# Kernel tuning notes

Measured on AMD Instinct MI355X. Metric: run time of the kernel, lower is better.

The kernel has to match this reference:

```python
import jax, jax.numpy as jnp
import numpy as np

N, L, S, H, D = 4, 2048, 2048, 8, 64

def setup_inputs() -> dict:
    key = jax.random.key(0)
    kq, kk, kv = jax.random.split(key, 3)
    queries = jax.random.normal(kq, (N, L, H, D), dtype=jnp.float32)
    keys = jax.random.normal(kk, (N, S, H, D), dtype=jnp.float32)
    values = jax.random.normal(kv, (N, S, H, D), dtype=jnp.float32)
    # q_mask all True (avoids NaN rows, matching torch semantics for valid queries);
    # kv_mask is a valid-prefix mask: first 3/4 of kv positions are valid.
    q_mask = jnp.ones((N, L), dtype=bool)
    kv_mask = jnp.arange(S)[None, :] < (S * 3 // 4)
    kv_mask = jnp.broadcast_to(kv_mask, (N, S))
    return {"queries": queries, "keys": keys, "values": values,
            "q_mask": q_mask, "kv_mask": kv_mask}

def reference(queries, keys, values, q_mask, kv_mask):
    # QK: [N, L, S, H]  (torch does broadcasted mul+sum; einsum is the same math)
    QK = jnp.einsum("nlhd,nshd->nlsh", queries, keys)
    mask = q_mask[:, :, None, None] & kv_mask[:, None, :, None]  # [N,L,S,1]
    QK = jnp.where(mask, QK, -jnp.inf)
    softmax_temp = 1.0 / jnp.sqrt(jnp.asarray(D, queries.dtype))
    A = jax.nn.softmax(softmax_temp * QK, axis=2)  # softmax over S
    # AV: [N, L, H, D]
    return jnp.einsum("nlsh,nshd->nlhd", A, values)
```

## Files before the change

### kernel.cpp

```cpp
#include <hip/hip_runtime.h>
#include <hip/hip_bf16.h>
#include <stdint.h>


namespace {

constexpr int N_ = 4, L_ = 2048, S_ = 2048, H_ = 8, D_ = 64;
constexpr int KVBLK = 64;
constexpr int NT = S_ / KVBLK;
constexpr int TILE_BYTES = 64 * 128;
constexpr float QSC = 0.125f * 1.44269504088896f;

typedef __bf16 bf16x8 __attribute__((ext_vector_type(8)));
typedef __bf16 bf16x4 __attribute__((ext_vector_type(4)));
typedef float f32x4 __attribute__((ext_vector_type(4)));

__device__ inline int swz(int row, int byte_in_row) {
    return row * 128 + (byte_in_row ^ ((row & 7) << 4));
}

__device__ inline bf16x8 cvt8(float4 a, float4 b) {
    bf16x8 r;
    r[0] = (__bf16)a.x; r[1] = (__bf16)a.y; r[2] = (__bf16)a.z; r[3] = (__bf16)a.w;
    r[4] = (__bf16)b.x; r[5] = (__bf16)b.y; r[6] = (__bf16)b.z; r[7] = (__bf16)b.w;
    return r;
}

__device__ inline void gl_lds16(const void* g, void* l) {
    __builtin_amdgcn_global_load_lds(
        (const __attribute__((address_space(1))) unsigned int*)g,
        (__attribute__((address_space(3))) unsigned int*)l, 16, 0, 0);
}

__global__ __launch_bounds__(256)
void prep_kernel(const float* __restrict__ K, const float* __restrict__ V,
                 uint8_t* __restrict__ Kimg, uint8_t* __restrict__ Vimg)
{
    const int bid = blockIdx.x;
    const int t   = bid & (NT - 1);
    const int nh  = bid >> 5;
    const int h   = nh & (H_ - 1);
    const int n   = nh / H_;
    const int tid = threadIdx.x;

    uint8_t* kt = Kimg + (size_t)bid * TILE_BYTES;
    uint8_t* vt = Vimg + (size_t)bid * TILE_BYTES;

    {
        const int r = tid >> 2, seg = tid & 3;
        const float* kp = K + (((size_t)n * S_ + t * 64 + r) * H_ + h) * D_ + seg * 16;
        float4 f0 = ((const float4*)kp)[0];
        float4 f1 = ((const float4*)kp)[1];
        float4 f2 = ((const float4*)kp)[2];
        float4 f3 = ((const float4*)kp)[3];
        *(bf16x8*)(kt + swz(r, seg * 32))      = cvt8(f0, f1);
        *(bf16x8*)(kt + swz(r, seg * 32 + 16)) = cvt8(f2, f3);
    }

    {
        const int vd = tid & 63, vw = tid >> 6;
        const float* vp = V + (((size_t)n * S_ + t * 64 + vw * 16) * H_ + h) * D_ + vd;
        #pragma unroll
        for (int i4 = 0; i4 < 4; ++i4) {
            bf16x4 u;
            u[0] = (__bf16)vp[(size_t)(i4 * 4 + 0) * (H_ * D_)];
            u[1] = (__bf16)vp[(size_t)(i4 * 4 + 1) * (H_ * D_)];
            u[2] = (__bf16)vp[(size_t)(i4 * 4 + 2) * (H_ * D_)];
            u[3] = (__bf16)vp[(size_t)(i4 * 4 + 3) * (H_ * D_)];
            *(bf16x4*)(vt + swz(vd, (vw * 16 + i4 * 4) * 2)) = u;
        }
    }
}

__global__ __launch_bounds__(128, 2)
void fa_kernel(const float* __restrict__ Q, const uint8_t* __restrict__ Kimg,
               const uint8_t* __restrict__ Vimg, const void* __restrict__ kvm_raw,
               float* __restrict__ O)
{
    const int b   = blockIdx.x;
    const int xcd = b & 7;
    const int k_  = b >> 3;
    const int nh  = xcd * 4 + (k_ >> 5);
    const int qt  = k_ & 31;
    const int h   = nh & (H_ - 1);
    const int n   = nh / H_;

    const int tid  = threadIdx.x;
    const int wave = tid >> 6;
    const int lane = tid & 63;
    const int lo   = lane & 15;
    const int hi   = lane >> 4;

    const int q0 = qt * 64 + wave * 32;

    __shared__ __align__(16) unsigned char Klds[2][TILE_BYTES];
    __shared__ __align__(16) unsigned char Vtld[2][TILE_BYTES];
    __shared__ __align__(16) unsigned char Plds[2][32 * 128];

    const uint8_t* k8  = (const uint8_t*)kvm_raw;
    const int*     k32 = (const int*)kvm_raw;
    const bool isb = (k8[1] | k8[2] | k8[3]) != 0;
    const size_t mbase = (size_t)n * S_;
    int cnt = 0;
    if (isb) {
        #pragma unroll
        for (int w = 0; w < 4; ++w) {
            uint2 v = *(const uint2*)(k8 + mbase + w * 512 + lane * 8);
            #pragma unroll
            for (int i = 0; i < 4; ++i) cnt += ((v.x >> (8 * i)) & 0xffu) ? 1 : 0;
            #pragma unroll
            for (int i = 0; i < 4; ++i) cnt += ((v.y >> (8 * i)) & 0xffu) ? 1 : 0;
        }
    } else {
        const int4* p = (const int4*)(k32 + mbase);
        #pragma unroll
        for (int w = 0; w < 4; ++w) {
            int4 a = p[w * 128 + lane * 2];
            int4 c = p[w * 128 + lane * 2 + 1];
            cnt += (a.x != 0) + (a.y != 0) + (a.z != 0) + (a.w != 0)
                 + (c.x != 0) + (c.y != 0) + (c.z != 0) + (c.w != 0);
        }
    }
    #pragma unroll
    for (int off = 1; off < 64; off <<= 1) cnt += __shfl_xor(cnt, off, 64);
    const int plen   = cnt;
    const int ntiles = (plen + KVBLK - 1) / KVBLK;

    bf16x8 qf[2][2];
    #pragma unroll
    for (int sub = 0; sub < 2; ++sub) {
        const float* qp = Q + (((size_t)n * L_ + q0 + sub * 16 + lo) * H_ + h) * D_;
        #pragma unroll
        for (int d0 = 0; d0 < 2; ++d0) {
            float4 a = *(const float4*)(qp + d0 * 32 + hi * 8);
            float4 c = *(const float4*)(qp + d0 * 32 + hi * 8 + 4);
            a.x *= QSC; a.y *= QSC; a.z *= QSC; a.w *= QSC;
            c.x *= QSC; c.y *= QSC; c.z *= QSC; c.w *= QSC;
            qf[sub][d0] = cvt8(a, c);
        }
    }

    bf16x8 ones8;
    #pragma unroll
    for (int j = 0; j < 8; ++j) ones8[j] = (__bf16)1.0f;

    f32x4 acc[2][4];
    f32x4 lacc[2];
    #pragma unroll
    for (int sub = 0; sub < 2; ++sub) {
        #pragma unroll
        for (int dt = 0; dt < 4; ++dt) acc[sub][dt] = f32x4{0.f, 0.f, 0.f, 0.f};
        lacc[sub] = f32x4{0.f, 0.f, 0.f, 0.f};
    }

    const uint8_t* kimg_nh = Kimg + (size_t)nh * NT * TILE_BYTES;
    const uint8_t* vimg_nh = Vimg + (size_t)nh * NT * TILE_BYTES;

    auto stage = [&](int buf, int t) {
        const uint8_t* kt = kimg_nh + (size_t)t * TILE_BYTES;
        const uint8_t* vt = vimg_nh + (size_t)t * TILE_BYTES;
        const int base = wave * 4096;
        #pragma unroll
        for (int i = 0; i < 4; ++i) {
            gl_lds16(kt + base + i * 1024 + lane * 16, &Klds[buf][base + i * 1024]);
            gl_lds16(vt + base + i * 1024 + lane * 16, &Vtld[buf][base + i * 1024]);
        }
    };

    if (ntiles > 0) stage(0, 0);

    for (int t = 0; t < ntiles; ++t) {
        const int buf = t & 1;
        const int s0 = t * KVBLK;

        __syncthreads();
        if (t + 1 < ntiles) stage(buf ^ 1, t + 1);

        f32x4 sacc[2][4];
        #pragma unroll
        for (int sub = 0; sub < 2; ++sub)
            #pragma unroll
            for (int nt = 0; nt < 4; ++nt) sacc[sub][nt] = f32x4{0.f, 0.f, 0.f, 0.f};
        #pragma unroll
        for (int nt = 0; nt < 4; ++nt) {
            #pragma unroll
            for (int d0 = 0; d0 < 2; ++d0) {
                const bf16x8 kb = *(const bf16x8*)(Klds[buf] + swz(nt * 16 + lo, d0 * 64 + hi * 16));
                sacc[0][nt] = __builtin_amdgcn_mfma_f32_16x16x32_bf16(qf[0][d0], kb, sacc[0][nt], 0, 0, 0);
                sacc[1][nt] = __builtin_amdgcn_mfma_f32_16x16x32_bf16(qf[1][d0], kb, sacc[1][nt], 0, 0, 0);
            }
        }

        #pragma unroll
        for (int sub = 0; sub < 2; ++sub) {
            #pragma unroll
            for (int nt = 0; nt < 4; ++nt) {
                const bool valid = (s0 + nt * 16 + lo) < plen;
                #pragma unroll
                for (int r = 0; r < 4; ++r) {
                    const float pv = valid ? __builtin_amdgcn_exp2f(sacc[sub][nt][r]) : 0.0f;
                    *(__bf16*)(Plds[wave] + swz(sub * 16 + hi * 4 + r, (nt * 16 + lo) * 2)) = (__bf16)pv;
                }
            }
        }

        #pragma unroll
        for (int kk = 0; kk < 2; ++kk) {
            const bf16x8 af0 = *(const bf16x8*)(Plds[wave] + swz(lo,      kk * 64 + hi * 16));
            const bf16x8 af1 = *(const bf16x8*)(Plds[wave] + swz(16 + lo, kk * 64 + hi * 16));
            lacc[0] = __builtin_amdgcn_mfma_f32_16x16x32_bf16(af0, ones8, lacc[0], 0, 0, 0);
            lacc[1] = __builtin_amdgcn_mfma_f32_16x16x32_bf16(af1, ones8, lacc[1], 0, 0, 0);
            #pragma unroll
            for (int dt = 0; dt < 4; ++dt) {
                const bf16x8 bfr = *(const bf16x8*)(Vtld[buf] + swz(dt * 16 + lo, kk * 64 + hi * 16));
                acc[0][dt] = __builtin_amdgcn_mfma_f32_16x16x32_bf16(af0, bfr, acc[0][dt], 0, 0, 0);
                acc[1][dt] = __builtin_amdgcn_mfma_f32_16x16x32_bf16(af1, bfr, acc[1][dt], 0, 0, 0);
            }
        }
    }

    #pragma unroll
    for (int sub = 0; sub < 2; ++sub) {
        #pragma unroll
        for (int r = 0; r < 4; ++r) {
            const float inv = lacc[sub][r] > 0.f ? 1.0f / lacc[sub][r] : 0.f;
            float* op = O + (((size_t)n * L_ + q0 + sub * 16 + hi * 4 + r) * H_ + h) * D_ + lo;
            #pragma unroll
            for (int dt = 0; dt < 4; ++dt)
                op[dt * 16] = acc[sub][dt][r] * inv;
        }
    }
}

}

extern "C" void kernel_launch(void* const* d_in, const int* in_sizes, int n_in,
                              void* d_out, int out_size, void* d_ws, size_t ws_size,
                              hipStream_t stream) {
    const float* Q = (const float*)d_in[0];
    const float* K = (const float*)d_in[1];
    const float* V = (const float*)d_in[2];
    const void* kvm = d_in[4];
    float* O = (float*)d_out;

    uint8_t* Kimg = (uint8_t*)d_ws;
    uint8_t* Vimg = Kimg + (size_t)N_ * H_ * NT * TILE_BYTES;

    prep_kernel<<<dim3(N_ * H_ * NT), dim3(256), 0, stream>>>(K, V, Kimg, Vimg);
    fa_kernel<<<dim3(N_ * H_ * NT), dim3(128), 0, stream>>>(Q, Kimg, Vimg, kvm, O);
}
```

Baseline: 144.8 us.

## Switch attention to 32x32x16 MFMA with register-resident P via permlane swap

Rewrites the attention inner loop to use 32x32x16 bf16 MFMAs computing S^T (K as the A operand), so the probabilities stay in registers. They are rearranged with v_permlane32_swap instead of a round trip through LDS. Row sums are accumulated in scalar registers rather than with an extra MFMA against a ones vector, and the exp masking is skipped for full tiles. The prep kernel lays out the K/V images in the fragment order the new MFMA expects, which removes the swizzle. This cuts LDS traffic and instruction count, at the cost of larger accumulator fragments and a shared-memory step to broadcast the row normalisation.

```diff
diff --git a/kernel.cpp b/kernel.cpp
--- a/kernel.cpp
+++ b/kernel.cpp
@@ -8,22 +8,24 @@
 constexpr int N_ = 4, L_ = 2048, S_ = 2048, H_ = 8, D_ = 64;
 constexpr int KVBLK = 64;
 constexpr int NT = S_ / KVBLK;
-constexpr int TILE_BYTES = 64 * 128;
+constexpr int TILE_BYTES = 64 * 64 * 2;
 constexpr float QSC = 0.125f * 1.44269504088896f;
 
 typedef __bf16 bf16x8 __attribute__((ext_vector_type(8)));
-typedef __bf16 bf16x4 __attribute__((ext_vector_type(4)));
-typedef float f32x4 __attribute__((ext_vector_type(4)));
-
-__device__ inline int swz(int row, int byte_in_row) {
-    return row * 128 + (byte_in_row ^ ((row & 7) << 4));
-}
+typedef __bf16 bf16x2 __attribute__((ext_vector_type(2)));
+typedef float  f32x16 __attribute__((ext_vector_type(16)));
+typedef unsigned int uint4v __attribute__((ext_vector_type(4)));
 
 __device__ inline bf16x8 cvt8(float4 a, float4 b) {
     bf16x8 r;
     r[0] = (__bf16)a.x; r[1] = (__bf16)a.y; r[2] = (__bf16)a.z; r[3] = (__bf16)a.w;
     r[4] = (__bf16)b.x; r[5] = (__bf16)b.y; r[6] = (__bf16)b.z; r[7] = (__bf16)b.w;
     return r;
+}
+
+__device__ inline uint32_t pack2(float a, float b) {
+    bf16x2 w; w[0] = (__bf16)a; w[1] = (__bf16)b;
+    return __builtin_bit_cast(uint32_t, w);
 }
 
 __device__ inline void gl_lds16(const void* g, void* l) {
@@ -40,35 +42,37 @@
     const int t   = bid & (NT - 1);
     const int nh  = bid >> 5;
     const int h   = nh & (H_ - 1);
-    const int n   = nh / H_;
+    const int n   = nh >> 3;
     const int tid = threadIdx.x;
 
     uint8_t* kt = Kimg + (size_t)bid * TILE_BYTES;
     uint8_t* vt = Vimg + (size_t)bid * TILE_BYTES;
 
     {
-        const int r = tid >> 2, seg = tid & 3;
-        const float* kp = K + (((size_t)n * S_ + t * 64 + r) * H_ + h) * D_ + seg * 16;
+        const int kv = tid & 63, dc = tid >> 6;
+        const int blk = kv >> 5, kv31 = kv & 31;
+        const float* kp = K + (((size_t)n * S_ + t * 64 + kv) * H_ + h) * D_ + dc * 16;
         float4 f0 = ((const float4*)kp)[0];
         float4 f1 = ((const float4*)kp)[1];
         float4 f2 = ((const float4*)kp)[2];
         float4 f3 = ((const float4*)kp)[3];
-        *(bf16x8*)(kt + swz(r, seg * 32))      = cvt8(f0, f1);
-        *(bf16x8*)(kt + swz(r, seg * 32 + 16)) = cvt8(f2, f3);
+        *(bf16x8*)(kt + ((blk * 4 + dc) * 64 + kv31) * 16)      = cvt8(f0, f1);
+        *(bf16x8*)(kt + ((blk * 4 + dc) * 64 + 32 + kv31) * 16) = cvt8(f2, f3);
     }
 
     {
-        const int vd = tid & 63, vw = tid >> 6;
-        const float* vp = V + (((size_t)n * S_ + t * 64 + vw * 16) * H_ + h) * D_ + vd;
-        #pragma unroll
-        for (int i4 = 0; i4 < 4; ++i4) {
-            bf16x4 u;
-            u[0] = (__bf16)vp[(size_t)(i4 * 4 + 0) * (H_ * D_)];
-            u[1] = (__bf16)vp[(size_t)(i4 * 4 + 1) * (H_ * D_)];
-            u[2] = (__bf16)vp[(size_t)(i4 * 4 + 2) * (H_ * D_)];
-            u[3] = (__bf16)vp[(size_t)(i4 * 4 + 3) * (H_ * D_)];
-            *(bf16x4*)(vt + swz(vd, (vw * 16 + i4 * 4) * 2)) = u;
-        }
+        const int d = tid & 63, kvg = tid >> 6;
+        const int dt = d >> 5, d31 = d & 31;
+        const int blk = kvg >> 1, c = kvg & 1;
+        const float* vp = V + (((size_t)n * S_ + t * 64 + kvg * 16) * H_ + h) * D_ + d;
+        bf16x8 u0, u1;
+        #pragma unroll
+        for (int j = 0; j < 8; ++j) u0[j] = (__bf16)vp[(size_t)j * (H_ * D_)];
+        #pragma unroll
+        for (int j = 0; j < 8; ++j) u1[j] = (__bf16)vp[(size_t)(8 + j) * (H_ * D_)];
+        const int cb = ((blk * 2 + c) * 2 + dt) * 64;
+        *(bf16x8*)(vt + (cb + d31) * 16)      = u0;
+        *(bf16x8*)(vt + (cb + 32 + d31) * 16) = u1;
     }
 }
 
@@ -83,19 +87,19 @@
     const int nh  = xcd * 4 + (k_ >> 5);
     const int qt  = k_ & 31;
     const int h   = nh & (H_ - 1);
-    const int n   = nh / H_;
+    const int n   = nh >> 3;
 
     const int tid  = threadIdx.x;
     const int wave = tid >> 6;
     const int lane = tid & 63;
-    const int lo   = lane & 15;
-    const int hi   = lane >> 4;
+    const int l31  = lane & 31;
+    const int hi5  = lane >> 5;
 
     const int q0 = qt * 64 + wave * 32;
 
-    __shared__ __align__(16) unsigned char Klds[2][TILE_BYTES];
-    __shared__ __align__(16) unsigned char Vtld[2][TILE_BYTES];
-    __shared__ __align__(16) unsigned char Plds[2][32 * 128];
+    __shared__ __align__(16) uint8_t Klds[2][TILE_BYTES];
+    __shared__ __align__(16) uint8_t Vlds[2][TILE_BYTES];
+    __shared__ float rinv[2][32];
 
     const uint8_t* k8  = (const uint8_t*)kvm_raw;
     const int*     k32 = (const int*)kvm_raw;
@@ -126,32 +130,25 @@
     const int plen   = cnt;
     const int ntiles = (plen + KVBLK - 1) / KVBLK;
 
-    bf16x8 qf[2][2];
-    #pragma unroll
-    for (int sub = 0; sub < 2; ++sub) {
-        const float* qp = Q + (((size_t)n * L_ + q0 + sub * 16 + lo) * H_ + h) * D_;
-        #pragma unroll
-        for (int d0 = 0; d0 < 2; ++d0) {
-            float4 a = *(const float4*)(qp + d0 * 32 + hi * 8);
-            float4 c = *(const float4*)(qp + d0 * 32 + hi * 8 + 4);
+    bf16x8 qf[4];
+    {
+        const float* qp = Q + (((size_t)n * L_ + q0 + l31) * H_ + h) * D_ + hi5 * 8;
+        #pragma unroll
+        for (int dc = 0; dc < 4; ++dc) {
+            float4 a = *(const float4*)(qp + dc * 16);
+            float4 c = *(const float4*)(qp + dc * 16 + 4);
             a.x *= QSC; a.y *= QSC; a.z *= QSC; a.w *= QSC;
             c.x *= QSC; c.y *= QSC; c.z *= QSC; c.w *= QSC;
-            qf[sub][d0] = cvt8(a, c);
-        }
-    }
-
-    bf16x8 ones8;
+            qf[dc] = cvt8(a, c);
+        }
+    }
+
+    f32x16 acc[2];
     #pragma unroll
-    for (int j = 0; j < 8; ++j) ones8[j] = (__bf16)1.0f;
-
-    f32x4 acc[2][4];
-    f32x4 lacc[2];
-    #pragma unroll
-    for (int sub = 0; sub < 2; ++sub) {
-        #pragma unroll
-        for (int dt = 0; dt < 4; ++dt) acc[sub][dt] = f32x4{0.f, 0.f, 0.f, 0.f};
-        lacc[sub] = f32x4{0.f, 0.f, 0.f, 0.f};
-    }
+    for (int dt = 0; dt < 2; ++dt)
+        #pragma unroll
+        for (int i = 0; i < 16; ++i) acc[dt][i] = 0.f;
+    float rs = 0.f;
 
     const uint8_t* kimg_nh = Kimg + (size_t)nh * NT * TILE_BYTES;
     const uint8_t* vimg_nh = Vimg + (size_t)nh * NT * TILE_BYTES;
@@ -163,7 +160,7 @@
         #pragma unroll
         for (int i = 0; i < 4; ++i) {
             gl_lds16(kt + base + i * 1024 + lane * 16, &Klds[buf][base + i * 1024]);
-            gl_lds16(vt + base + i * 1024 + lane * 16, &Vtld[buf][base + i * 1024]);
+            gl_lds16(vt + base + i * 1024 + lane * 16, &Vlds[buf][base + i * 1024]);
         }
     };
 
@@ -176,59 +173,68 @@
         __syncthreads();
         if (t + 1 < ntiles) stage(buf ^ 1, t + 1);
 
-        f32x4 sacc[2][4];
-        #pragma unroll
-        for (int sub = 0; sub < 2; ++sub)
-            #pragma unroll
-            for (int nt = 0; nt < 4; ++nt) sacc[sub][nt] = f32x4{0.f, 0.f, 0.f, 0.f};
-        #pragma unroll
-        for (int nt = 0; nt < 4; ++nt) {
-            #pragma unroll
-            for (int d0 = 0; d0 < 2; ++d0) {
-                const bf16x8 kb = *(const bf16x8*)(Klds[buf] + swz(nt * 16 + lo, d0 * 64 + hi * 16));
-                sacc[0][nt] = __builtin_amdgcn_mfma_f32_16x16x32_bf16(qf[0][d0], kb, sacc[0][nt], 0, 0, 0);
-                sacc[1][nt] = __builtin_amdgcn_mfma_f32_16x16x32_bf16(qf[1][d0], kb, sacc[1][nt], 0, 0, 0);
-            }
-        }
-
-        #pragma unroll
-        for (int sub = 0; sub < 2; ++sub) {
-            #pragma unroll
-            for (int nt = 0; nt < 4; ++nt) {
-                const bool valid = (s0 + nt * 16 + lo) < plen;
+        const bool full = (s0 + KVBLK) <= plen;
+
+        #pragma unroll
+        for (int blk = 0; blk < 2; ++blk) {
+            f32x16 sacc;
+            #pragma unroll
+            for (int i = 0; i < 16; ++i) sacc[i] = 0.f;
+            #pragma unroll
+            for (int dc = 0; dc < 4; ++dc) {
+                const bf16x8 ka = *(const bf16x8*)(&Klds[buf][(blk * 4 + dc) * 1024 + lane * 16]);
+                sacc = __builtin_amdgcn_mfma_f32_32x32x16_bf16(ka, qf[dc], sacc, 0, 0, 0);
+            }
+
+            float p[16];
+            if (full) {
                 #pragma unroll
-                for (int r = 0; r < 4; ++r) {
-                    const float pv = valid ? __builtin_amdgcn_exp2f(sacc[sub][nt][r]) : 0.0f;
-                    *(__bf16*)(Plds[wave] + swz(sub * 16 + hi * 4 + r, (nt * 16 + lo) * 2)) = (__bf16)pv;
+                for (int r = 0; r < 16; ++r) p[r] = __builtin_amdgcn_exp2f(sacc[r]);
+            } else {
+                const int kvb = s0 + blk * 32 + hi5 * 4;
+                #pragma unroll
+                for (int r = 0; r < 16; ++r) {
+                    const int kv = kvb + (r & 3) + 8 * (r >> 2);
+                    p[r] = (kv < plen) ? __builtin_amdgcn_exp2f(sacc[r]) : 0.f;
                 }
             }
-        }
-
-        #pragma unroll
-        for (int kk = 0; kk < 2; ++kk) {
-            const bf16x8 af0 = *(const bf16x8*)(Plds[wave] + swz(lo,      kk * 64 + hi * 16));
-            const bf16x8 af1 = *(const bf16x8*)(Plds[wave] + swz(16 + lo, kk * 64 + hi * 16));
-            lacc[0] = __builtin_amdgcn_mfma_f32_16x16x32_bf16(af0, ones8, lacc[0], 0, 0, 0);
-            lacc[1] = __builtin_amdgcn_mfma_f32_16x16x32_bf16(af1, ones8, lacc[1], 0, 0, 0);
-            #pragma unroll
-            for (int dt = 0; dt < 4; ++dt) {
-                const bf16x8 bfr = *(const bf16x8*)(Vtld[buf] + swz(dt * 16 + lo, kk * 64 + hi * 16));
-                acc[0][dt] = __builtin_amdgcn_mfma_f32_16x16x32_bf16(af0, bfr, acc[0][dt], 0, 0, 0);
-                acc[1][dt] = __builtin_amdgcn_mfma_f32_16x16x32_bf16(af1, bfr, acc[1][dt], 0, 0, 0);
-            }
-        }
-    }
-
+            #pragma unroll
+            for (int r = 0; r < 16; ++r) rs += p[r];
+
+            uint32_t W[4][2];
+            #pragma unroll
+            for (int cb = 0; cb < 4; ++cb) {
+                W[cb][0] = pack2(p[cb * 4 + 0], p[cb * 4 + 1]);
+                W[cb][1] = pack2(p[cb * 4 + 2], p[cb * 4 + 3]);
+            }
+
+            #pragma unroll
+            for (int c = 0; c < 2; ++c) {
+                uint32_t x0 = W[2 * c][0], y0 = W[2 * c + 1][0];
+                uint32_t x1 = W[2 * c][1], y1 = W[2 * c + 1][1];
+                asm volatile("v_permlane32_swap_b32 %0, %1" : "+v"(x0), "+v"(y0));
+                asm volatile("v_permlane32_swap_b32 %0, %1" : "+v"(x1), "+v"(y1));
+                uint4v fw; fw[0] = x0; fw[1] = x1; fw[2] = y0; fw[3] = y1;
+                const bf16x8 af = __builtin_bit_cast(bf16x8, fw);
+                #pragma unroll
+                for (int dt = 0; dt < 2; ++dt) {
+                    const bf16x8 vb = *(const bf16x8*)(
+                        &Vlds[buf][(((blk * 2 + c) * 2 + dt) * 1024) + lane * 16]);
+                    acc[dt] = __builtin_amdgcn_mfma_f32_32x32x16_bf16(af, vb, acc[dt], 0, 0, 0);
+                }
+            }
+        }
+    }
+
+    float rtot = rs + __shfl_xor(rs, 32, 64);
+    if (hi5 == 0) rinv[wave][l31] = rtot > 0.f ? 1.0f / rtot : 0.f;
     #pragma unroll
-    for (int sub = 0; sub < 2; ++sub) {
-        #pragma unroll
-        for (int r = 0; r < 4; ++r) {
-            const float inv = lacc[sub][r] > 0.f ? 1.0f / lacc[sub][r] : 0.f;
-            float* op = O + (((size_t)n * L_ + q0 + sub * 16 + hi * 4 + r) * H_ + h) * D_ + lo;
-            #pragma unroll
-            for (int dt = 0; dt < 4; ++dt)
-                op[dt * 16] = acc[sub][dt][r] * inv;
-        }
+    for (int rr = 0; rr < 16; ++rr) {
+        const int row = (rr & 3) + 8 * (rr >> 2) + 4 * hi5;
+        const float inv = rinv[wave][row];
+        float* op = O + (((size_t)n * L_ + q0 + row) * H_ + h) * D_ + l31;
+        op[0]  = acc[0][rr] * inv;
+        op[32] = acc[1][rr] * inv;
     }
 }
 
```

Measured after the change: 134.4 us. 1.08x faster.
